# Kernel tuning notes

Hardware: AMD Instinct MI355X
Metric: run time of the kernel (lower is better)

## Reference

```python
import jax, jax.numpy as jnp
import numpy as np

N = 50000   # num nodes
D = 64      # feature dim
E = 800000  # num edges (avg degree 16)


def setup_inputs() -> dict:
    key = jax.random.key(0)
    k1, k2, k3 = jax.random.split(key, 3)
    x = jax.random.normal(k1, (N, D), dtype=jnp.float32)
    edge_index = jax.random.randint(k2, (2, E), 0, N, dtype=jnp.int32)
    edge_weight = jax.random.uniform(k3, (E,), dtype=jnp.float32)
    return {"x": x, "edge_index": edge_index, "edge_weight": edge_weight}


def reference(x, edge_index, edge_weight):
    """Faithful translation of scatter_median (spmm with reduce='median'):
    per destination node, the (lower) median over its weighted incoming
    neighbor messages, computed independently per feature channel.
    Nodes with zero in-degree produce zeros (as in the torch code where
    h is initialized to zeros and degree-0 rows are skipped).
    """
    n, d = x.shape
    e = edge_index.shape[1]

    # sort edges by destination (stable sort; within-segment order is irrelevant for median)
    order = jnp.argsort(edge_index[1])
    row = edge_index[0, order]
    col = edge_index[1, order]
    w = edge_weight[order]

    # weighted messages: x_j = x[row] * w  -> [E, D]
    x_j = x[row] * w[:, None]

    # per-destination degree and position of each edge within its segment
    deg = jnp.bincount(col, length=n)                                   # [N]
    starts = jnp.concatenate([jnp.zeros(1, deg.dtype), jnp.cumsum(deg)[:-1]])
    pos = jnp.arange(e, dtype=deg.dtype) - starts[col]                  # [E]

    # dense batch [N, max_deg, D], padded with +inf so pads sort to the end
    max_deg = int(jnp.max(deg))  # concrete on materialized inputs
    dense = jnp.full((n, max_deg, d), jnp.inf, dtype=x.dtype)
    dense = dense.at[col, pos].set(x_j)

    # per-channel sort, then pick the lower-median index (torch.median semantics:
    # for even counts it returns the lower of the two middle values)
    dense = jnp.sort(dense, axis=1)
    idx = jnp.maximum((deg - 1) // 2, 0)                                # [N]
    med = jnp.take_along_axis(dense, idx[:, None, None], axis=1)[:, 0]  # [N, D]

    return jnp.where(deg[:, None] > 0, med, jnp.zeros((), dtype=x.dtype))
```

## Files before the change

kernel.cpp:

```cpp
#include <hip/hip_runtime.h>
#include <stdint.h>
#include <math.h>

#define NN 50000
#define DD 64
#define EE 800000
#define BSZ 64
#define NB 782
#define BCAP 1280
#define EPW 4096
#define CAP 48


__global__ void zero_cnt(int* __restrict__ cnt) {
    int i = blockIdx.x * blockDim.x + threadIdx.x;
    if (i < NB) cnt[i] = 0;
}

__global__ __launch_bounds__(512) void bucketize(
        const int* __restrict__ ei, const float* __restrict__ ew,
        int* __restrict__ bucket_cnt, uint64_t* __restrict__ recs) {
    __shared__ int   hist[NB];
    __shared__ int   base[NB];
    __shared__ int   eL[EPW];
    __shared__ int   dL[EPW];
    __shared__ float wL[EPW];
    const int t = threadIdx.x;
    const int e0 = blockIdx.x * EPW;
    const int nE = (e0 + EPW < EE) ? EPW : (EE - e0);

    for (int i = t; i < NB; i += 512) hist[i] = 0;
    for (int i = t; i < nE; i += 512) {
        eL[i] = ei[e0 + i];
        dL[i] = ei[EE + e0 + i];
        wL[i] = ew[e0 + i];
    }
    __syncthreads();

    for (int i = t; i < nE; i += 512)
        atomicAdd(&hist[dL[i] >> 6], 1);
    __syncthreads();

    for (int i = t; i < NB; i += 512) {
        int c = hist[i];
        base[i] = (c > 0) ? atomicAdd(&bucket_cnt[i], c) : 0;
        hist[i] = 0;
    }
    __syncthreads();

    for (int i = t; i < nE; i += 512) {
        int d = dL[i];
        int b = d >> 6;
        int p = base[b] + atomicAdd(&hist[b], 1);
        if (p < BCAP)
            recs[(size_t)b * BCAP + p] =
                ((uint64_t)__float_as_uint(wL[i]) << 32) |
                ((uint32_t)eL[i] << 6) | (uint32_t)(d & 63);
    }
}

__global__ __launch_bounds__(256) void bin_dense(
        const int* __restrict__ bucket_cnt, const uint64_t* __restrict__ recs,
        uint64_t* __restrict__ slots, int* __restrict__ deg) {
    __shared__ uint64_t sl[BSZ * CAP];
    __shared__ int degl[BSZ];
    const int t = threadIdx.x;
    const int b = blockIdx.x;

    int cnt = bucket_cnt[b];
    if (cnt > BCAP) cnt = BCAP;

    for (int i = t; i < BSZ; i += 256) degl[i] = 0;
    __syncthreads();

    const uint64_t* br = recs + (size_t)b * BCAP;
    for (int i = t; i < cnt; i += 256) {
        uint64_t r = br[i];
        int loc = (int)(r & 63u);
        int p = atomicAdd(&degl[loc], 1);
        if (p < CAP)
            sl[loc * CAP + p] = (r & 0xFFFFFFFF00000000ull)
                              | (uint32_t)(((uint32_t)r) >> 6);
    }
    __syncthreads();

    uint64_t* outrow = slots + (size_t)b * BSZ * CAP;
    for (int i = t; i < BSZ * CAP; i += 256) outrow[i] = sl[i];
    int n0 = b * BSZ;
    for (int i = t; i < BSZ; i += 256)
        if (n0 + i < NN) deg[n0 + i] = degl[i];
}

__device__ __forceinline__ void cswap(float& a, float& b) {
    float lo = fminf(a, b);
    float hi = fmaxf(a, b);
    a = lo; b = hi;
}

template<int I, int END, int R, int STEP, int PW>
struct Pairs {
    static __device__ __forceinline__ void run(float (&r)[PW]) {
        if constexpr (I + R < END) {
            cswap(r[I], r[I + R]);
            Pairs<I + STEP, END, R, STEP, PW>::run(r);
        }
    }
};

template<int LO, int N, int R, int PW>
struct Merge {
    static __device__ __forceinline__ void run(float (&r)[PW]) {
        if constexpr (2 * R < N) {
            Merge<LO,     N, 2 * R, PW>::run(r);
            Merge<LO + R, N, 2 * R, PW>::run(r);
            Pairs<LO + R, LO + N, R, 2 * R, PW>::run(r);
        } else {
            cswap(r[LO], r[LO + R]);
        }
    }
};

template<int LO, int N, int PW>
struct Sorter {
    static __device__ __forceinline__ void run(float (&r)[PW]) {
        if constexpr (N > 1) {
            Sorter<LO,         N / 2, PW>::run(r);
            Sorter<LO + N / 2, N / 2, PW>::run(r);
            Merge<LO, N, 1, PW>::run(r);
        }
    }
};

template <int PW>
__device__ __forceinline__ float gather_sort_u(const float* __restrict__ x, int lane,
                                               int dg, int k,
                                               const uint64_t* __restrict__ row) {
    float r[PW];
    #pragma unroll
    for (int j = 0; j < PW; ++j) {
        float v = INFINITY;
        if (j < dg) {
            uint64_t s = row[j];
            uint32_t src = (uint32_t)(s & 0xffffffffu);
            float    w   = __uint_as_float((uint32_t)(s >> 32));
            v = x[(size_t)src * DD + lane] * w;
        }
        r[j] = v;
    }
    Sorter<0, PW, PW>::run(r);
    constexpr int KLO = PW / 4;
    constexpr int KHI = (PW / 2 > 0) ? PW / 2 - 1 : 0;
    float med = r[KLO];
    #pragma unroll
    for (int t = KLO + 1; t <= KHI; ++t)
        if (t == k) med = r[t];
    return med;
}

__global__ __launch_bounds__(256, 4) void median_kernel(
    const float* __restrict__ x, const int* __restrict__ deg,
    const uint64_t* __restrict__ slots, float* __restrict__ out) {
    const int lane = threadIdx.x & 63;
    int n = blockIdx.x * 4 + (threadIdx.x >> 6);
    n = __builtin_amdgcn_readfirstlane(n);
    if (n >= NN) return;

    int dg = __builtin_amdgcn_readfirstlane(deg[n]);
    if (dg > CAP) dg = CAP;
    if (dg == 0) { out[(size_t)n * DD + lane] = 0.f; return; }

    const uint64_t* row = slots + (size_t)n * CAP;
    const int k = (dg - 1) >> 1;
    float med;

    if      (dg <= 2)  med = gather_sort_u<2>(x, lane, dg, k, row);
    else if (dg <= 4)  med = gather_sort_u<4>(x, lane, dg, k, row);
    else if (dg <= 8)  med = gather_sort_u<8>(x, lane, dg, k, row);
    else if (dg <= 16) med = gather_sort_u<16>(x, lane, dg, k, row);
    else if (dg <= 32) med = gather_sort_u<32>(x, lane, dg, k, row);
    else               med = gather_sort_u<64>(x, lane, dg, k, row);

    out[(size_t)n * DD + lane] = med;
}

extern "C" void kernel_launch(void* const* d_in, const int* in_sizes, int n_in,
                              void* d_out, int out_size, void* d_ws, size_t ws_size,
                              hipStream_t stream) {
    const float*  x  = (const float*)d_in[0];
    const int*    ei = (const int*)d_in[1];
    const float*  ew = (const float*)d_in[2];
    float* out = (float*)d_out;

    int*      bucket_cnt = (int*)d_ws;
    int*      deg        = (int*)((char*)d_ws + (1 << 14));
    uint64_t* recs       = (uint64_t*)((char*)d_ws + (1 << 18));
    uint64_t* slots      = (uint64_t*)((char*)d_ws + (1 << 23));

    zero_cnt<<<(NB + 255) / 256, 256, 0, stream>>>(bucket_cnt);
    bucketize<<<(EE + EPW - 1) / EPW, 512, 0, stream>>>(ei, ew, bucket_cnt, recs);
    bin_dense<<<NB, 256, 0, stream>>>(bucket_cnt, recs, slots, deg);
    median_kernel<<<(NN + 3) / 4, 256, 0, stream>>>(x, deg, slots, out);
}
```

Measured before the change: 136.8 us.

## Software-pipeline median gather with persistent waves and split rare high-degree nodes

The median kernel becomes a persistent grid-stride kernel that double-buffers register arrays, so the gather for the next node is issued before the current node is sorted. This is meant to hide gather latency behind the sorting network. Nodes with degree above 32 are listed during binning and handled by a separate small kernel, which keeps the main kernel's register arrays at 32 entries. The cost is higher register pressure from two 32-float buffers, which may reduce occupancy, plus an extra kernel launch and an atomic counter.

```diff
diff --git a/kernel.cpp b/kernel.cpp
--- a/kernel.cpp
+++ b/kernel.cpp
@@ -10,11 +10,12 @@
 #define BCAP 1280
 #define EPW 4096
 #define CAP 48
+#define BIGMAX 1024
 
 
 __global__ void zero_cnt(int* __restrict__ cnt) {
     int i = blockIdx.x * blockDim.x + threadIdx.x;
-    if (i < NB) cnt[i] = 0;
+    if (i < NB + 1) cnt[i] = 0;
 }
 
 __global__ __launch_bounds__(512) void bucketize(
@@ -61,7 +62,8 @@
 
 __global__ __launch_bounds__(256) void bin_dense(
         const int* __restrict__ bucket_cnt, const uint64_t* __restrict__ recs,
-        uint64_t* __restrict__ slots, int* __restrict__ deg) {
+        uint64_t* __restrict__ slots, int* __restrict__ deg,
+        int* __restrict__ big_cnt, int* __restrict__ big_list) {
     __shared__ uint64_t sl[BSZ * CAP];
     __shared__ int degl[BSZ];
     const int t = threadIdx.x;
@@ -87,8 +89,18 @@
     uint64_t* outrow = slots + (size_t)b * BSZ * CAP;
     for (int i = t; i < BSZ * CAP; i += 256) outrow[i] = sl[i];
     int n0 = b * BSZ;
-    for (int i = t; i < BSZ; i += 256)
-        if (n0 + i < NN) deg[n0 + i] = degl[i];
+    for (int i = t; i < BSZ; i += 256) {
+        int n = n0 + i;
+        if (n < NN) {
+            int dgi = degl[i];
+            if (dgi > CAP) dgi = CAP;
+            deg[n] = dgi;
+            if (dgi > 32) {
+                int q = atomicAdd(big_cnt, 1);
+                if (q < BIGMAX) big_list[q] = n;
+            }
+        }
+    }
 }
 
 __device__ __forceinline__ void cswap(float& a, float& b) {
@@ -97,57 +109,44 @@
     a = lo; b = hi;
 }
 
-template<int I, int END, int R, int STEP, int PW>
+template<int I, int END, int R, int STEP, int AW>
 struct Pairs {
-    static __device__ __forceinline__ void run(float (&r)[PW]) {
+    static __device__ __forceinline__ void run(float (&r)[AW]) {
         if constexpr (I + R < END) {
             cswap(r[I], r[I + R]);
-            Pairs<I + STEP, END, R, STEP, PW>::run(r);
+            Pairs<I + STEP, END, R, STEP, AW>::run(r);
         }
     }
 };
 
-template<int LO, int N, int R, int PW>
+template<int LO, int N, int R, int AW>
 struct Merge {
-    static __device__ __forceinline__ void run(float (&r)[PW]) {
+    static __device__ __forceinline__ void run(float (&r)[AW]) {
         if constexpr (2 * R < N) {
-            Merge<LO,     N, 2 * R, PW>::run(r);
-            Merge<LO + R, N, 2 * R, PW>::run(r);
-            Pairs<LO + R, LO + N, R, 2 * R, PW>::run(r);
+            Merge<LO,     N, 2 * R, AW>::run(r);
+            Merge<LO + R, N, 2 * R, AW>::run(r);
+            Pairs<LO + R, LO + N, R, 2 * R, AW>::run(r);
         } else {
             cswap(r[LO], r[LO + R]);
         }
     }
 };
 
-template<int LO, int N, int PW>
+template<int LO, int N, int AW>
 struct Sorter {
-    static __device__ __forceinline__ void run(float (&r)[PW]) {
+    static __device__ __forceinline__ void run(float (&r)[AW]) {
         if constexpr (N > 1) {
-            Sorter<LO,         N / 2, PW>::run(r);
-            Sorter<LO + N / 2, N / 2, PW>::run(r);
-            Merge<LO, N, 1, PW>::run(r);
+            Sorter<LO,         N / 2, AW>::run(r);
+            Sorter<LO + N / 2, N / 2, AW>::run(r);
+            Merge<LO, N, 1, AW>::run(r);
         }
     }
 };
 
 template <int PW>
-__device__ __forceinline__ float gather_sort_u(const float* __restrict__ x, int lane,
-                                               int dg, int k,
-                                               const uint64_t* __restrict__ row) {
-    float r[PW];
-    #pragma unroll
-    for (int j = 0; j < PW; ++j) {
-        float v = INFINITY;
-        if (j < dg) {
-            uint64_t s = row[j];
-            uint32_t src = (uint32_t)(s & 0xffffffffu);
-            float    w   = __uint_as_float((uint32_t)(s >> 32));
-            v = x[(size_t)src * DD + lane] * w;
-        }
-        r[j] = v;
-    }
-    Sorter<0, PW, PW>::run(r);
+__device__ __forceinline__ float sortsel(float (&r)[32], int dg) {
+    Sorter<0, PW, 32>::run(r);
+    const int k = (dg - 1) >> 1;
     constexpr int KLO = PW / 4;
     constexpr int KHI = (PW / 2 > 0) ? PW / 2 - 1 : 0;
     float med = r[KLO];
@@ -157,30 +156,109 @@
     return med;
 }
 
-__global__ __launch_bounds__(256, 4) void median_kernel(
+
+__device__ __forceinline__ int stageA(const float* __restrict__ x,
+                                      const int* __restrict__ deg,
+                                      const uint64_t* __restrict__ slots,
+                                      int lane, int n, float (&r)[32], int& dg_out) {
+    int dg = __builtin_amdgcn_readfirstlane(deg[n]);
+    dg_out = dg;
+    int dgc = (dg > 32) ? 0 : dg;
+    const uint64_t* row = slots + (size_t)n * CAP;
+    #pragma unroll
+    for (int j = 0; j < 32; ++j) {
+        float v = INFINITY;
+        if (j < dgc) {
+            uint64_t s = row[j];
+            uint32_t src = (uint32_t)(s & 0xffffffffu);
+            float    w   = __uint_as_float((uint32_t)(s >> 32));
+            v = x[(size_t)src * DD + lane] * w;
+        }
+        r[j] = v;
+    }
+    return dgc;
+}
+
+__device__ __forceinline__ void stageB(int lane, int n, int dg, float (&r)[32],
+                                       float* __restrict__ out) {
+    if (dg > 32) return;
+    float med = 0.f;
+    if (dg > 0) {
+        if      (dg <= 2)  med = sortsel<2>(r, dg);
+        else if (dg <= 4)  med = sortsel<4>(r, dg);
+        else if (dg <= 8)  med = sortsel<8>(r, dg);
+        else if (dg <= 16) med = sortsel<16>(r, dg);
+        else               med = sortsel<32>(r, dg);
+    }
+    out[(size_t)n * DD + lane] = med;
+}
+
+__global__ __launch_bounds__(256, 4) void median_main(
     const float* __restrict__ x, const int* __restrict__ deg,
     const uint64_t* __restrict__ slots, float* __restrict__ out) {
     const int lane = threadIdx.x & 63;
-    int n = blockIdx.x * 4 + (threadIdx.x >> 6);
-    n = __builtin_amdgcn_readfirstlane(n);
+    const int wid  = (blockIdx.x * blockDim.x + threadIdx.x) >> 6;
+    const int S    = (gridDim.x * blockDim.x) >> 6;
+
+    float rA[32], rB[32];
+    int dgA, dgB;
+
+    int n = wid;
     if (n >= NN) return;
-
-    int dg = __builtin_amdgcn_readfirstlane(deg[n]);
-    if (dg > CAP) dg = CAP;
-    if (dg == 0) { out[(size_t)n * DD + lane] = 0.f; return; }
-
-    const uint64_t* row = slots + (size_t)n * CAP;
-    const int k = (dg - 1) >> 1;
-    float med;
-
-    if      (dg <= 2)  med = gather_sort_u<2>(x, lane, dg, k, row);
-    else if (dg <= 4)  med = gather_sort_u<4>(x, lane, dg, k, row);
-    else if (dg <= 8)  med = gather_sort_u<8>(x, lane, dg, k, row);
-    else if (dg <= 16) med = gather_sort_u<16>(x, lane, dg, k, row);
-    else if (dg <= 32) med = gather_sort_u<32>(x, lane, dg, k, row);
-    else               med = gather_sort_u<64>(x, lane, dg, k, row);
-
-    out[(size_t)n * DD + lane] = med;
+    stageA(x, deg, slots, lane, n, rA, dgA);
+    int nA = n; n += S;
+
+    while (n < NN) {
+        stageA(x, deg, slots, lane, n, rB, dgB);
+        int nB = n; n += S;
+        stageB(lane, nA, dgA, rA, out);
+        if (n < NN) {
+            stageA(x, deg, slots, lane, n, rA, dgA);
+            nA = n; n += S;
+            stageB(lane, nB, dgB, rB, out);
+        } else {
+            stageB(lane, nB, dgB, rB, out);
+            return;
+        }
+    }
+    stageB(lane, nA, dgA, rA, out);
+}
+
+__global__ __launch_bounds__(256) void median_big(
+    const float* __restrict__ x, const int* __restrict__ deg,
+    const uint64_t* __restrict__ slots, const int* __restrict__ big_cnt,
+    const int* __restrict__ big_list, float* __restrict__ out) {
+    const int lane = threadIdx.x & 63;
+    const int wid  = (blockIdx.x * blockDim.x + threadIdx.x) >> 6;
+    const int S    = (gridDim.x * blockDim.x) >> 6;
+
+    int cnt = __builtin_amdgcn_readfirstlane(big_cnt[0]);
+    if (cnt > BIGMAX) cnt = BIGMAX;
+
+    for (int i = wid; i < cnt; i += S) {
+        int n  = __builtin_amdgcn_readfirstlane(big_list[i]);
+        int dg = __builtin_amdgcn_readfirstlane(deg[n]);
+        const uint64_t* row = slots + (size_t)n * CAP;
+        float r[64];
+        #pragma unroll
+        for (int j = 0; j < 64; ++j) {
+            float v = INFINITY;
+            if (j < dg) {
+                uint64_t s = row[j];
+                uint32_t src = (uint32_t)(s & 0xffffffffu);
+                float    w   = __uint_as_float((uint32_t)(s >> 32));
+                v = x[(size_t)src * DD + lane] * w;
+            }
+            r[j] = v;
+        }
+        Sorter<0, 64, 64>::run(r);
+        const int k = (dg - 1) >> 1;
+        float med = r[16];
+        #pragma unroll
+        for (int t = 17; t <= 31; ++t)
+            if (t == k) med = r[t];
+        out[(size_t)n * DD + lane] = med;
+    }
 }
 
 extern "C" void kernel_launch(void* const* d_in, const int* in_sizes, int n_in,
@@ -192,12 +270,15 @@
     float* out = (float*)d_out;
 
     int*      bucket_cnt = (int*)d_ws;
+    int*      big_cnt    = bucket_cnt + NB;
+    int*      big_list   = (int*)((char*)d_ws + (1 << 12));
     int*      deg        = (int*)((char*)d_ws + (1 << 14));
     uint64_t* recs       = (uint64_t*)((char*)d_ws + (1 << 18));
     uint64_t* slots      = (uint64_t*)((char*)d_ws + (1 << 23));
 
-    zero_cnt<<<(NB + 255) / 256, 256, 0, stream>>>(bucket_cnt);
+    zero_cnt<<<(NB + 1 + 255) / 256, 256, 0, stream>>>(bucket_cnt);
     bucketize<<<(EE + EPW - 1) / EPW, 512, 0, stream>>>(ei, ew, bucket_cnt, recs);
-    bin_dense<<<NB, 256, 0, stream>>>(bucket_cnt, recs, slots, deg);
-    median_kernel<<<(NN + 3) / 4, 256, 0, stream>>>(x, deg, slots, out);
-}
+    bin_dense<<<NB, 256, 0, stream>>>(bucket_cnt, recs, slots, deg, big_cnt, big_list);
+    median_main<<<2048, 256, 0, stream>>>(x, deg, slots, out);
+    median_big<<<16, 256, 0, stream>>>(x, deg, slots, big_cnt, big_list, out);
+}
```

New measurement: 244.5 us. +78.8%, slower.
